# Kernel tuning notes

Hardware: AMD Instinct MI355X
Metric: run time of the kernel (lower is better)

Reference implementation:

```python
import jax, jax.numpy as jnp
import numpy as np

Bb, H, L = 4, 512, 4096      # batch, d_model, seq len
N2 = 32                       # d_state//2 complex conjugate-pair modes
Cch = 1                       # channels
DM = 512                      # d_model (output dim)

def setup_inputs() -> dict:
    key = jax.random.key(0)
    ks = jax.random.split(key, 8)
    u = jax.random.normal(ks[0], (Bb, H, L), jnp.float32)
    # dt ~ LogUniform[1e-3, 1e-1] as in S4 defaults
    log_dt = (jax.random.uniform(ks[1], (H,), jnp.float32)
              * (np.log(0.1) - np.log(0.001)) + np.log(0.001)).astype(jnp.float32)
    # S4D-Lin initialization: A = -1/2 + i*pi*n
    A_re = -0.5 * jnp.ones((H, N2), jnp.float32)
    A_im = jnp.broadcast_to(np.pi * jnp.arange(N2, dtype=np.float32), (H, N2)).astype(jnp.float32)
    B_re = jnp.ones((H, N2), jnp.float32)
    B_im = jnp.zeros((H, N2), jnp.float32)
    C_re = jax.random.normal(ks[2], (Cch, H, N2), jnp.float32) * (N2 ** -0.5)
    C_im = jax.random.normal(ks[3], (Cch, H, N2), jnp.float32) * (N2 ** -0.5)
    D = jax.random.normal(ks[4], (Cch, H), jnp.float32)
    W_out = jax.random.normal(ks[5], (2 * DM, Cch * H), jnp.float32) * ((Cch * H) ** -0.5)
    b_out = jnp.zeros((2 * DM,), jnp.float32)
    return {"u": u, "log_dt": log_dt, "A_re": A_re, "A_im": A_im,
            "B_re": B_re, "B_im": B_im, "C_re": C_re, "C_im": C_im,
            "D": D, "W_out": W_out, "b_out": b_out}

def reference(u, log_dt, A_re, A_im, B_re, B_im, C_re, C_im, D, W_out, b_out):
    # --- SSM kernel generation (diag / S4D, ZOH discretization) ---
    dt = jnp.exp(log_dt)                      # (H,)
    A = A_re + 1j * A_im                      # (H, N2)
    Bc = B_re + 1j * B_im                     # (H, N2)
    Cc = C_re + 1j * C_im                     # (C, H, N2)
    dtA = dt[:, None] * A                     # (H, N2)
    dB = (jnp.exp(dtA) - 1.0) / A * Bc        # (H, N2)
    pos = jnp.arange(L, dtype=jnp.float32)
    V = jnp.exp(dtA[:, :, None] * pos)        # (H, N2, L) Vandermonde of dA^l
    # factor 2 accounts for conjugate-pair halves
    k = (2.0 * jnp.einsum('chn,hn,hnl->chl', Cc, dB, V).real).astype(u.dtype)  # (C,H,L)
    # --- FFT convolution: y = k * u (causal, linear conv via zero-padded FFT) ---
    n_fft = 2 * L
    k_f = jnp.fft.rfft(k, n=n_fft)            # (C, H, L+1)
    u_f = jnp.fft.rfft(u, n=n_fft)            # (B, H, L+1)
    y_f = jnp.einsum('bhl,chl->bchl', u_f, k_f)
    y = jnp.fft.irfft(y_f, n=n_fft)[..., :L]  # (B, C, H, L)
    # skip connection D
    y = y + jnp.einsum('bhl,ch->bchl', u, D)
    y = y.reshape(u.shape[0], Cch * H, L)     # 'b c h l -> b (c h) l'
    # pointwise activation (exact GELU, matching torch default)
    y = jax.nn.gelu(y, approximate=False)
    # output linear (transposed, kernel-size-1) + GLU over channel dim
    z = jnp.einsum('bhl,oh->bol', y, W_out) + b_out[None, :, None]  # (B, 2*DM, L)
    out = z[:, :DM] * jax.nn.sigmoid(z[:, DM:])                      # (B, DM, L)
    return out
```

## Files before the change

### kernel.cpp

```cpp
#include <hip/hip_runtime.h>
#include <math.h>

#define BB 4
#define HH 512
#define LL 4096
#define NN 32
#define DMOUT 512

typedef __attribute__((ext_vector_type(8))) short short8;
typedef __attribute__((ext_vector_type(4))) float f32x4;

__device__ __forceinline__ unsigned f2bf(float x) {
    unsigned u = __float_as_uint(x);
    return (u + 0x7fffu + ((u >> 16) & 1u)) >> 16;
}
__device__ __forceinline__ unsigned packhl(float x) {
    unsigned hb = f2bf(x);
    float xh = __uint_as_float(hb << 16);
    return (hb << 16) | f2bf(x - xh);
}
__device__ __forceinline__ float reconhl(unsigned v) {
    return __uint_as_float(v & 0xffff0000u) + __uint_as_float(v << 16);
}
__device__ __forceinline__ void gload_lds16(const void* g, void* l) {
    __builtin_amdgcn_global_load_lds((const __attribute__((address_space(1))) void*)g,
                                     (__attribute__((address_space(3))) void*)l, 16, 0, 0);
}

__global__ void wsplit_kernel(const float* __restrict__ W, unsigned short* __restrict__ whi) {
    int i = (blockIdx.x * 256 + threadIdx.x) * 4;
    float4 w = *(const float4*)(W + i);
    ushort4 o;
    o.x = (unsigned short)f2bf(w.x);
    o.y = (unsigned short)f2bf(w.y);
    o.z = (unsigned short)f2bf(w.z);
    o.w = (unsigned short)f2bf(w.w);
    *(ushort4*)(whi + i) = o;
}

__global__ __launch_bounds__(256) void prep_kernel(
    const float* __restrict__ log_dt,
    const float* __restrict__ A_re, const float* __restrict__ A_im,
    const float* __restrict__ B_re, const float* __restrict__ B_im,
    const float* __restrict__ C_re, const float* __restrict__ C_im,
    unsigned* __restrict__ A3t, unsigned* __restrict__ Et) {
    const int h = blockIdx.x;
    const int tid = threadIdx.x;
    __shared__ float cst_lds[256];

    if (tid < 32) {
        int n = tid;
        float dt = expf(log_dt[h]);
        float ar = A_re[h * NN + n], ai = A_im[h * NN + n];
        float dtar = dt * ar, dtai = dt * ai;
        float ea = expf(dtar);
        float s, c; sincosf(dtai, &s, &c);
        float dA_r = ea * c, dA_i = ea * s;
        float em_r = dA_r - 1.0f, em_i = dA_i;
        float inv = 1.0f / (ar * ar + ai * ai);
        float t_r = (em_r * ar + em_i * ai) * inv;
        float t_i = (em_i * ar - em_r * ai) * inv;
        float br = B_re[h * NN + n], bi = B_im[h * NN + n];
        cst_lds[0 * 32 + n] = dtar;
        cst_lds[1 * 32 + n] = dtai;
        cst_lds[2 * 32 + n] = dA_r;
        cst_lds[3 * 32 + n] = dA_i;
        cst_lds[4 * 32 + n] = t_r * br - t_i * bi;
        cst_lds[5 * 32 + n] = t_r * bi + t_i * br;
        cst_lds[6 * 32 + n] = 2.0f * C_re[h * NN + n];
        cst_lds[7 * 32 + n] = 2.0f * C_im[h * NN + n];
    }
    __syncthreads();

    const int n = tid & 31, q = tid >> 5;
    const float dtar = cst_lds[0 * 32 + n], dtai = cst_lds[1 * 32 + n];
    const float dAr = cst_lds[2 * 32 + n], dAi = cst_lds[3 * 32 + n];
    const float dbr = cst_lds[4 * 32 + n], dbi = cst_lds[5 * 32 + n];
    const float tcr = cst_lds[6 * 32 + n], tci = cst_lds[7 * 32 + n];

    {
        float p = (float)(56 - q * 8);
        float mr = expf(p * dtar);
        float s, c; sincosf(p * dtai, &s, &c);
        float pr = mr * c, pi = mr * s;
        unsigned* base = A3t + (size_t)h * 4096;
#pragma unroll
        for (int jj = 7; jj >= 0; jj--) {
            int m = q * 8 + jj;
            base[m * 64 + n]      = packhl(dbr * pr - dbi * pi);
            base[m * 64 + 32 + n] = packhl(dbr * pi + dbi * pr);
            float nr2 = pr * dAr - pi * dAi;
            pi = pr * dAi + pi * dAr;
            pr = nr2;
        }
    }
    {
        float p = (float)(q * 8 + 1);
        float mr = expf(p * dtar);
        float s, c; sincosf(p * dtai, &s, &c);
        float pr = mr * c, pi = mr * s;
        unsigned* base = Et + (size_t)h * 4096;
#pragma unroll
        for (int i = q * 8; i <= q * 8 + 7; i++) {
            base[i * 64 + n]      = packhl(tcr * pr - tci * pi);
            base[i * 64 + 32 + n] = packhl(-(tcr * pi + tci * pr));
            float nr2 = pr * dAr - pi * dAi;
            pi = pr * dAi + pi * dAr;
            pr = nr2;
        }
    }
}

__global__ __launch_bounds__(256, 4) void ssm_kernel(
    const float* __restrict__ u, const float* __restrict__ log_dt,
    const float* __restrict__ A_re, const float* __restrict__ A_im,
    const float* __restrict__ B_re, const float* __restrict__ B_im,
    const float* __restrict__ C_re, const float* __restrict__ C_im,
    const float* __restrict__ D,
    const unsigned* __restrict__ A3t, const unsigned* __restrict__ Et,
    unsigned short* __restrict__ yhi) {
    const int h = blockIdx.x;
    const int b = blockIdx.y;
    const int tid = threadIdx.x;
    const int lane = tid & 63;
    const int w = tid >> 6;
    const int g = lane >> 4;
    const int l15 = lane & 15;

    __shared__ unsigned short uh[64 * 72];
    __shared__ unsigned short ul[64 * 72];
    __shared__ unsigned XsR[32 * 65];
    __shared__ unsigned XsI[32 * 65];
    __shared__ unsigned karr_pk[128];
    __shared__ float kpart[256];
    __shared__ float cst_lds[256];

    {
        const float* urow = u + ((size_t)(b * HH + h)) * LL;
#pragma unroll
        for (int r = 0; r < 4; r++) {
            int f = tid + 256 * r;
            float4 v = *(const float4*)(urow + f * 4);
            int t = f >> 4, mb = (f & 15) << 2;
            unsigned hx = f2bf(v.x), hy = f2bf(v.y), hz = f2bf(v.z), hw = f2bf(v.w);
            uint2 hwv;
            hwv.x = hx | (hy << 16);
            hwv.y = hz | (hw << 16);
            float rx = v.x - __uint_as_float(hx << 16);
            float ry = v.y - __uint_as_float(hy << 16);
            float rz = v.z - __uint_as_float(hz << 16);
            float rw = v.w - __uint_as_float(hw << 16);
            uint2 lwv;
            lwv.x = f2bf(rx) | (f2bf(ry) << 16);
            lwv.y = f2bf(rz) | (f2bf(rw) << 16);
            *(uint2*)(&uh[t * 72 + mb]) = hwv;
            *(uint2*)(&ul[t * 72 + mb]) = lwv;
        }
    }
    if (tid < 32) {
        int n = tid;
        float dt = expf(log_dt[h]);
        float ar = A_re[h * NN + n], ai = A_im[h * NN + n];
        float dtar = dt * ar, dtai = dt * ai;
        float ea = expf(dtar);
        float s, c; sincosf(dtai, &s, &c);
        float dA_r = ea * c, dA_i = ea * s;
        float em_r = dA_r - 1.0f, em_i = dA_i;
        float inv = 1.0f / (ar * ar + ai * ai);
        float t_r = (em_r * ar + em_i * ai) * inv;
        float t_i = (em_i * ar - em_r * ai) * inv;
        float br = B_re[h * NN + n], bi = B_im[h * NN + n];
        cst_lds[0 * 32 + n] = dtar;
        cst_lds[1 * 32 + n] = dtai;
        cst_lds[2 * 32 + n] = dA_r;
        cst_lds[3 * 32 + n] = dA_i;
        cst_lds[4 * 32 + n] = t_r * br - t_i * bi;
        cst_lds[5 * 32 + n] = t_r * bi + t_i * br;
        cst_lds[6 * 32 + n] = 2.0f * C_re[h * NN + n];
        cst_lds[7 * 32 + n] = 2.0f * C_im[h * NN + n];
    }
    __syncthreads();

    {
        int nprime = w * 16 + l15;
        const unsigned* a3b = A3t + (size_t)h * 4096 + nprime;
        short8 a3h0, a3l0, a3h1, a3l1;
#pragma unroll
        for (int j = 0; j < 8; j++) {
            unsigned v = a3b[(g * 8 + j) * 64];
            a3h0[j] = (short)(v >> 16); a3l0[j] = (short)(v & 0xffffu);
            unsigned v2 = a3b[(32 + g * 8 + j) * 64];
            a3h1[j] = (short)(v2 >> 16); a3l1[j] = (short)(v2 & 0xffffu);
        }
#pragma unroll
        for (int ni = 0; ni < 4; ni++) {
            int t = ni * 16 + l15;
            short8 uH0 = *(const short8*)(uh + t * 72 + g * 8);
            short8 uL0 = *(const short8*)(ul + t * 72 + g * 8);
            short8 uH1 = *(const short8*)(uh + t * 72 + 32 + g * 8);
            short8 uL1 = *(const short8*)(ul + t * 72 + 32 + g * 8);
            f32x4 a = (f32x4){0.f, 0.f, 0.f, 0.f};
            a = __builtin_amdgcn_mfma_f32_16x16x32_bf16(a3h0, uH0, a, 0, 0, 0);
            a = __builtin_amdgcn_mfma_f32_16x16x32_bf16(a3l0, uH0, a, 0, 0, 0);
            a = __builtin_amdgcn_mfma_f32_16x16x32_bf16(a3h0, uL0, a, 0, 0, 0);
            a = __builtin_amdgcn_mfma_f32_16x16x32_bf16(a3h1, uH1, a, 0, 0, 0);
            a = __builtin_amdgcn_mfma_f32_16x16x32_bf16(a3l1, uH1, a, 0, 0, 0);
            a = __builtin_amdgcn_mfma_f32_16x16x32_bf16(a3h1, uL1, a, 0, 0, 0);
            int nprime2 = w * 16 + g * 4;
#pragma unroll
            for (int r = 0; r < 4; r++) {
                int nn2 = nprime2 + r;
                if (nn2 < 32) XsR[nn2 * 65 + t] = __float_as_uint(a[r]);
                else          XsI[(nn2 - 32) * 65 + t] = __float_as_uint(a[r]);
            }
        }
    }
    {
        int j = tid & 63, nr = tid >> 6;
        float acc = 0.0f;
        if (j == 0) {
#pragma unroll
            for (int q = 0; q < 8; q++) {
                int n = nr * 8 + q;
                acc = fmaf(cst_lds[6 * 32 + n], cst_lds[4 * 32 + n], acc);
                acc = fmaf(-cst_lds[7 * 32 + n], cst_lds[5 * 32 + n], acc);
            }
        } else {
            const unsigned* eb = Et + (size_t)h * 4096 + (j - 1) * 64;
#pragma unroll
            for (int q = 0; q < 8; q++) {
                int n = nr * 8 + q;
                acc = fmaf(reconhl(eb[n]), cst_lds[4 * 32 + n], acc);
                acc = fmaf(reconhl(eb[32 + n]), cst_lds[5 * 32 + n], acc);
            }
        }
        kpart[nr * 64 + j] = acc;
    }
    __syncthreads();

    if (tid < 32) {
        int n = tid;
        float dtar = cst_lds[0 * 32 + n], dtai = cst_lds[1 * 32 + n];
        float mr = expf(64.0f * dtar);
        float s, c; sincosf(64.0f * dtai, &s, &c);
        float Mr = mr * c, Mi = mr * s;
        float cr = 0.f, ci = 0.f;
        unsigned* pR = XsR + n * 65;
        unsigned* pI = XsI + n * 65;
        float fr = __uint_as_float(pR[0]);
        float fi2 = __uint_as_float(pI[0]);
#pragma unroll 4
        for (int t = 0; t < 64; t++) {
            float frn = 0.f, fin = 0.f;
            if (t < 63) { frn = __uint_as_float(pR[t + 1]); fin = __uint_as_float(pI[t + 1]); }
            pR[t] = packhl(cr);
            pI[t] = packhl(ci);
            float nr = fmaf(Mr, cr, fmaf(-Mi, ci, fr));
            float nic = fmaf(Mr, ci, fmaf(Mi, cr, fi2));
            cr = nr; ci = nic;
            fr = frn; fi2 = fin;
        }
    } else if (tid >= 64 && tid < 128) {
        int j = tid - 64;
        float k = kpart[j] + kpart[64 + j] + kpart[128 + j] + kpart[192 + j];
        karr_pk[64 + j] = packhl(k);
    } else if (tid >= 128 && tid < 192) {
        karr_pk[tid - 128] = 0u;
    }
    __syncthreads();

    {
        int i = w * 16 + l15;
        short8 kh0, kl0, kh1, kl1;
#pragma unroll
        for (int j = 0; j < 8; j++) {
            unsigned v0 = karr_pk[64 + i - (g * 8 + j)];
            kh0[j] = (short)(v0 >> 16); kl0[j] = (short)(v0 & 0xffffu);
            unsigned v1 = karr_pk[64 + i - (32 + g * 8 + j)];
            kh1[j] = (short)(v1 >> 16); kl1[j] = (short)(v1 & 0xffffu);
        }
        short8 e0h, e0l, e1h, e1l;
        {
            const unsigned* eb = Et + (size_t)h * 4096 + i * 64;
#pragma unroll
            for (int j = 0; j < 8; j++) {
                int n = g * 8 + j;
                unsigned v = eb[n];
                e0h[j] = (short)(v >> 16); e0l[j] = (short)(v & 0xffffu);
                unsigned v2 = eb[32 + n];
                e1h[j] = (short)(v2 >> 16); e1l[j] = (short)(v2 & 0xffffu);
            }
        }
        float Dh = D[h];
        unsigned short* orow = yhi + ((size_t)(b * HH + h)) * LL;
#pragma unroll
        for (int ni = 0; ni < 4; ni++) {
            int t = ni * 16 + l15;
            short8 uH0 = *(const short8*)(uh + t * 72 + g * 8);
            short8 uL0 = *(const short8*)(ul + t * 72 + g * 8);
            short8 uH1 = *(const short8*)(uh + t * 72 + 32 + g * 8);
            short8 uL1 = *(const short8*)(ul + t * 72 + 32 + g * 8);
            short8 xrh, xrl, xih, xil;
#pragma unroll
            for (int j = 0; j < 8; j++) {
                unsigned v = XsR[(g * 8 + j) * 65 + t];
                xrh[j] = (short)(v >> 16); xrl[j] = (short)(v & 0xffffu);
                unsigned v2 = XsI[(g * 8 + j) * 65 + t];
                xih[j] = (short)(v2 >> 16); xil[j] = (short)(v2 & 0xffffu);
            }
            f32x4 a = (f32x4){0.f, 0.f, 0.f, 0.f};
            a = __builtin_amdgcn_mfma_f32_16x16x32_bf16(kh0, uH0, a, 0, 0, 0);
            a = __builtin_amdgcn_mfma_f32_16x16x32_bf16(kl0, uH0, a, 0, 0, 0);
            a = __builtin_amdgcn_mfma_f32_16x16x32_bf16(kh0, uL0, a, 0, 0, 0);
            a = __builtin_amdgcn_mfma_f32_16x16x32_bf16(kh1, uH1, a, 0, 0, 0);
            a = __builtin_amdgcn_mfma_f32_16x16x32_bf16(kl1, uH1, a, 0, 0, 0);
            a = __builtin_amdgcn_mfma_f32_16x16x32_bf16(kh1, uL1, a, 0, 0, 0);
            a = __builtin_amdgcn_mfma_f32_16x16x32_bf16(e0h, xrh, a, 0, 0, 0);
            a = __builtin_amdgcn_mfma_f32_16x16x32_bf16(e0h, xrl, a, 0, 0, 0);
            a = __builtin_amdgcn_mfma_f32_16x16x32_bf16(e0l, xrh, a, 0, 0, 0);
            a = __builtin_amdgcn_mfma_f32_16x16x32_bf16(e1h, xih, a, 0, 0, 0);
            a = __builtin_amdgcn_mfma_f32_16x16x32_bf16(e1h, xil, a, 0, 0, 0);
            a = __builtin_amdgcn_mfma_f32_16x16x32_bf16(e1l, xih, a, 0, 0, 0);
            ushort4 ov;
            unsigned short* op = &ov.x;
#pragma unroll
            for (int r = 0; r < 4; r++) {
                int io = w * 16 + g * 4 + r;
                float uv = __uint_as_float(((unsigned)uh[t * 72 + io]) << 16)
                         + __uint_as_float(((unsigned)ul[t * 72 + io]) << 16);
                float y = a[r] + Dh * uv;
                float gl = 0.5f * y * (1.0f + erff(y * 0.70710678118654752f));
                op[r] = (unsigned short)f2bf(gl);
            }
            *(ushort4*)(&orow[t * 64 + w * 16 + g * 4]) = ov;
        }
    }
}

__global__ __launch_bounds__(256) void gemm_glu_mfma(const unsigned short* __restrict__ yhi,
                                                     const float* __restrict__ W,
                                                     const unsigned short* __restrict__ whi,
                                                     const float* __restrict__ bias,
                                                     float* __restrict__ out, int preW) {
    const int b = blockIdx.z;
    const int d0 = blockIdx.y * 64;
    const int l0 = blockIdx.x * 64;
    const int tid = threadIdx.x;
    const int lane = tid & 63;
    const int wid = tid >> 6;
    const int wave_m = wid & 1;
    const int wave_n = wid >> 1;
    const int l15 = lane & 15;
    const int g = lane >> 4;

    __shared__ unsigned short Ysh[32 * 64];
    __shared__ char Wlds[128 * 64];

    f32x4 acc[4][2];
#pragma unroll
    for (int i = 0; i < 4; i++)
#pragma unroll
        for (int j = 0; j < 2; j++) acc[i][j] = (f32x4){0.f, 0.f, 0.f, 0.f};

    for (int kt = 0; kt < 16; kt++) {
        const int h0 = kt * 32;
        __syncthreads();
        {
            int kr = tid >> 3;
            int cc = tid & 7;
            int scol = (cc * 8) ^ ((kr & 8) ? 8 : 0);
            const unsigned short* src = yhi + ((size_t)(b * HH + h0 + kr)) * LL + l0 + scol;
            gload_lds16(src, (char*)Ysh + tid * 16);
        }
        if (preW) {
#pragma unroll
            for (int e = 0; e < 2; e++) {
                int c = e * 256 + tid;
                int row = c >> 2;
                int gx = c & 3;
                int qq = (row >> 1) & 3;
                int grow = (row < 64) ? (d0 + row) : (448 + d0 + row);
                const unsigned short* src = whi + (size_t)grow * 512 + h0 + ((gx ^ qq) * 8);
                gload_lds16(src, Wlds + c * 16);
            }
        } else {
            int row = tid >> 1;
            int kb = (tid & 1) * 16;
            int qq = (row >> 1) & 3;
            int grow = (row < 64) ? (d0 + row) : (448 + d0 + row);
            const float* src = W + (size_t)grow * 512 + h0 + kb;
            float4 w0 = *(const float4*)(src);
            float4 w1 = *(const float4*)(src + 4);
            float4 w2 = *(const float4*)(src + 8);
            float4 w3 = *(const float4*)(src + 12);
            short8 v0, v1;
            v0[0] = (short)f2bf(w0.x); v0[1] = (short)f2bf(w0.y);
            v0[2] = (short)f2bf(w0.z); v0[3] = (short)f2bf(w0.w);
            v0[4] = (short)f2bf(w1.x); v0[5] = (short)f2bf(w1.y);
            v0[6] = (short)f2bf(w1.z); v0[7] = (short)f2bf(w1.w);
            v1[0] = (short)f2bf(w2.x); v1[1] = (short)f2bf(w2.y);
            v1[2] = (short)f2bf(w2.z); v1[3] = (short)f2bf(w2.w);
            v1[4] = (short)f2bf(w3.x); v1[5] = (short)f2bf(w3.y);
            v1[6] = (short)f2bf(w3.z); v1[7] = (short)f2bf(w3.w);
            int g0 = kb >> 3;
            *(short8*)(Wlds + row * 64 + ((g0 ^ qq) * 16)) = v0;
            *(short8*)(Wlds + row * 64 + (((g0 + 1) ^ qq) * 16)) = v1;
        }
        __syncthreads();

        short8 af[4];
#pragma unroll
        for (int mi = 0; mi < 4; mi++) {
            int rowb = (mi < 2) ? (wave_m * 32 + mi * 16) : (64 + wave_m * 32 + (mi - 2) * 16);
            int row = rowb + l15;
            int qq = (row >> 1) & 3;
            af[mi] = *(const short8*)(Wlds + row * 64 + ((g ^ qq) * 16));
        }
#pragma unroll
        for (int ni = 0; ni < 2; ni++) {
            int col = wave_n * 32 + ni * 16 + l15;
            int cs = col ^ ((g & 1) << 3);
            const unsigned short* yb = Ysh + (8 * g) * 64 + cs;
            short8 bh;
            bh[0] = (short)yb[0 * 64];
            bh[1] = (short)yb[1 * 64];
            bh[2] = (short)yb[2 * 64];
            bh[3] = (short)yb[3 * 64];
            bh[4] = (short)yb[4 * 64];
            bh[5] = (short)yb[5 * 64];
            bh[6] = (short)yb[6 * 64];
            bh[7] = (short)yb[7 * 64];
#pragma unroll
            for (int mi = 0; mi < 4; mi++) {
                acc[mi][ni] = __builtin_amdgcn_mfma_f32_16x16x32_bf16(af[mi], bh, acc[mi][ni], 0, 0, 0);
            }
        }
    }

#pragma unroll
    for (int mi = 0; mi < 2; mi++) {
        int dbase = d0 + wave_m * 32 + mi * 16 + (g << 2);
#pragma unroll
        for (int r = 0; r < 4; r++) {
            int d = dbase + r;
            float b1 = bias[d], b2 = bias[DMOUT + d];
#pragma unroll
            for (int ni = 0; ni < 2; ni++) {
                int l = l0 + wave_n * 32 + ni * 16 + l15;
                float z1 = acc[mi][ni][r] + b1;
                float z2 = acc[mi + 2][ni][r] + b2;
                out[((size_t)(b * DMOUT + d)) * LL + l] = z1 * (1.0f / (1.0f + expf(-z2)));
            }
        }
    }
}

extern "C" void kernel_launch(void* const* d_in, const int* in_sizes, int n_in,
                              void* d_out, int out_size, void* d_ws, size_t ws_size,
                              hipStream_t stream) {
    const float* u      = (const float*)d_in[0];
    const float* log_dt = (const float*)d_in[1];
    const float* A_re   = (const float*)d_in[2];
    const float* A_im   = (const float*)d_in[3];
    const float* B_re   = (const float*)d_in[4];
    const float* B_im   = (const float*)d_in[5];
    const float* C_re   = (const float*)d_in[6];
    const float* C_im   = (const float*)d_in[7];
    const float* D      = (const float*)d_in[8];
    const float* W      = (const float*)d_in[9];
    const float* bias   = (const float*)d_in[10];
    float* out = (float*)d_out;

    char* ws = (char*)d_ws;
    unsigned short* yhi = (unsigned short*)ws;
    unsigned* A3t = (unsigned*)(ws + 16777216);
    unsigned* Et  = (unsigned*)(ws + 16777216 + 8388608);
    unsigned short* whi = (unsigned short*)(ws + 33554432);
    int preW = (ws_size >= (size_t)(33554432 + 1048576)) ? 1 : 0;

    if (preW) wsplit_kernel<<<512, 256, 0, stream>>>(W, whi);
    prep_kernel<<<HH, 256, 0, stream>>>(log_dt, A_re, A_im, B_re, B_im, C_re, C_im, A3t, Et);
    ssm_kernel<<<dim3(HH, BB), 256, 0, stream>>>(u, log_dt, A_re, A_im, B_re, B_im,
                                                 C_re, C_im, D, A3t, Et, yhi);
    gemm_glu_mfma<<<dim3(64, 8, BB), 256, 0, stream>>>(yhi, W, whi, bias, out, preW);
}
```

Baseline: 92.32 us.

## Double-buffer GEMM LDS tiles, fold W conversion into prep, hoist Et loads

The GEMM+GLU kernel now double-buffers its Y and W shared-memory tiles, issuing the next k-tile's async global-to-LDS loads before computing on the current one, with one barrier per iteration instead of two. The separate W-to-bf16 conversion kernel is merged into prep_kernel, which saves one launch. In the SSM kernel, the Et fragment loads are hoisted above a barrier so their latency overlaps other work. The cost is doubled LDS use in the GEMM, which may lower occupancy, and more live registers in the SSM kernel.

```diff
diff --git a/kernel.cpp b/kernel.cpp
--- a/kernel.cpp
+++ b/kernel.cpp
@@ -27,26 +27,28 @@
                                      (__attribute__((address_space(3))) void*)l, 16, 0, 0);
 }
 
-__global__ void wsplit_kernel(const float* __restrict__ W, unsigned short* __restrict__ whi) {
-    int i = (blockIdx.x * 256 + threadIdx.x) * 4;
-    float4 w = *(const float4*)(W + i);
-    ushort4 o;
-    o.x = (unsigned short)f2bf(w.x);
-    o.y = (unsigned short)f2bf(w.y);
-    o.z = (unsigned short)f2bf(w.z);
-    o.w = (unsigned short)f2bf(w.w);
-    *(ushort4*)(whi + i) = o;
-}
-
 __global__ __launch_bounds__(256) void prep_kernel(
     const float* __restrict__ log_dt,
     const float* __restrict__ A_re, const float* __restrict__ A_im,
     const float* __restrict__ B_re, const float* __restrict__ B_im,
     const float* __restrict__ C_re, const float* __restrict__ C_im,
-    unsigned* __restrict__ A3t, unsigned* __restrict__ Et) {
+    const float* __restrict__ W,
+    unsigned* __restrict__ A3t, unsigned* __restrict__ Et,
+    unsigned short* __restrict__ whi, int preW) {
     const int h = blockIdx.x;
     const int tid = threadIdx.x;
     __shared__ float cst_lds[256];
+
+    if (preW) {
+        int i = (h * 256 + tid) * 4;
+        float4 wv = *(const float4*)(W + i);
+        ushort4 o;
+        o.x = (unsigned short)f2bf(wv.x);
+        o.y = (unsigned short)f2bf(wv.y);
+        o.z = (unsigned short)f2bf(wv.z);
+        o.w = (unsigned short)f2bf(wv.w);
+        *(ushort4*)(whi + i) = o;
+    }
 
     if (tid < 32) {
         int n = tid;
@@ -236,6 +238,19 @@
         }
         kpart[nr * 64 + j] = acc;
     }
+    short8 e0h, e0l, e1h, e1l;
+    {
+        int i = w * 16 + l15;
+        const unsigned* eb = Et + (size_t)h * 4096 + i * 64;
+#pragma unroll
+        for (int j = 0; j < 8; j++) {
+            int n = g * 8 + j;
+            unsigned v = eb[n];
+            e0h[j] = (short)(v >> 16); e0l[j] = (short)(v & 0xffffu);
+            unsigned v2 = eb[32 + n];
+            e1h[j] = (short)(v2 >> 16); e1l[j] = (short)(v2 & 0xffffu);
+        }
+    }
     __syncthreads();
 
     if (tid < 32) {
@@ -279,18 +294,6 @@
             unsigned v1 = karr_pk[64 + i - (32 + g * 8 + j)];
             kh1[j] = (short)(v1 >> 16); kl1[j] = (short)(v1 & 0xffffu);
         }
-        short8 e0h, e0l, e1h, e1l;
-        {
-            const unsigned* eb = Et + (size_t)h * 4096 + i * 64;
-#pragma unroll
-            for (int j = 0; j < 8; j++) {
-                int n = g * 8 + j;
-                unsigned v = eb[n];
-                e0h[j] = (short)(v >> 16); e0l[j] = (short)(v & 0xffffu);
-                unsigned v2 = eb[32 + n];
-                e1h[j] = (short)(v2 >> 16); e1l[j] = (short)(v2 & 0xffffu);
-            }
-        }
         float Dh = D[h];
         unsigned short* orow = yhi + ((size_t)(b * HH + h)) * LL;
 #pragma unroll
@@ -353,8 +356,8 @@
     const int l15 = lane & 15;
     const int g = lane >> 4;
 
-    __shared__ unsigned short Ysh[32 * 64];
-    __shared__ char Wlds[128 * 64];
+    __shared__ unsigned short Ysh[2][32 * 64];
+    __shared__ char Wlds[2][128 * 64];
 
     f32x4 acc[4][2];
 #pragma unroll
@@ -362,51 +365,58 @@
 #pragma unroll
         for (int j = 0; j < 2; j++) acc[i][j] = (f32x4){0.f, 0.f, 0.f, 0.f};
 
+#define STAGE(BUF, KT)                                                                   \
+    {                                                                                    \
+        const int h0s = (KT) * 32;                                                       \
+        {                                                                                \
+            int kr = tid >> 3;                                                           \
+            int cc = tid & 7;                                                            \
+            int scol = (cc * 8) ^ ((kr & 8) ? 8 : 0);                                    \
+            const unsigned short* srcY = yhi + ((size_t)(b * HH + h0s + kr)) * LL + l0 + scol; \
+            gload_lds16(srcY, (char*)Ysh[BUF] + tid * 16);                               \
+        }                                                                                \
+        if (preW) {                                                                      \
+            _Pragma("unroll")                                                            \
+            for (int e = 0; e < 2; e++) {                                                \
+                int c = e * 256 + tid;                                                   \
+                int row = c >> 2;                                                        \
+                int gx = c & 3;                                                          \
+                int qq = (row >> 1) & 3;                                                 \
+                int grow = (row < 64) ? (d0 + row) : (448 + d0 + row);                   \
+                const unsigned short* srcW = whi + (size_t)grow * 512 + h0s + ((gx ^ qq) * 8); \
+                gload_lds16(srcW, Wlds[BUF] + c * 16);                                   \
+            }                                                                            \
+        } else {                                                                         \
+            int row = tid >> 1;                                                          \
+            int kb = (tid & 1) * 16;                                                     \
+            int qq = (row >> 1) & 3;                                                     \
+            int grow = (row < 64) ? (d0 + row) : (448 + d0 + row);                       \
+            const float* srcW = W + (size_t)grow * 512 + h0s + kb;                       \
+            float4 w0 = *(const float4*)(srcW);                                          \
+            float4 w1 = *(const float4*)(srcW + 4);                                      \
+            float4 w2 = *(const float4*)(srcW + 8);                                      \
+            float4 w3 = *(const float4*)(srcW + 12);                                     \
+            short8 v0, v1;                                                               \
+            v0[0] = (short)f2bf(w0.x); v0[1] = (short)f2bf(w0.y);                        \
+            v0[2] = (short)f2bf(w0.z); v0[3] = (short)f2bf(w0.w);                        \
+            v0[4] = (short)f2bf(w1.x); v0[5] = (short)f2bf(w1.y);                        \
+            v0[6] = (short)f2bf(w1.z); v0[7] = (short)f2bf(w1.w);                        \
+            v1[0] = (short)f2bf(w2.x); v1[1] = (short)f2bf(w2.y);                        \
+            v1[2] = (short)f2bf(w2.z); v1[3] = (short)f2bf(w2.w);                        \
+            v1[4] = (short)f2bf(w3.x); v1[5] = (short)f2bf(w3.y);                        \
+            v1[6] = (short)f2bf(w3.z); v1[7] = (short)f2bf(w3.w);                        \
+            int g0 = kb >> 3;                                                            \
+            *(short8*)(Wlds[BUF] + row * 64 + ((g0 ^ qq) * 16)) = v0;                    \
+            *(short8*)(Wlds[BUF] + row * 64 + (((g0 + 1) ^ qq) * 16)) = v1;              \
+        }                                                                                \
+    }
+
+    STAGE(0, 0)
+    __syncthreads();
+
+    int cur = 0;
     for (int kt = 0; kt < 16; kt++) {
-        const int h0 = kt * 32;
-        __syncthreads();
-        {
-            int kr = tid >> 3;
-            int cc = tid & 7;
-            int scol = (cc * 8) ^ ((kr & 8) ? 8 : 0);
-            const unsigned short* src = yhi + ((size_t)(b * HH + h0 + kr)) * LL + l0 + scol;
-            gload_lds16(src, (char*)Ysh + tid * 16);
-        }
-        if (preW) {
-#pragma unroll
-            for (int e = 0; e < 2; e++) {
-                int c = e * 256 + tid;
-                int row = c >> 2;
-                int gx = c & 3;
-                int qq = (row >> 1) & 3;
-                int grow = (row < 64) ? (d0 + row) : (448 + d0 + row);
-                const unsigned short* src = whi + (size_t)grow * 512 + h0 + ((gx ^ qq) * 8);
-                gload_lds16(src, Wlds + c * 16);
-            }
-        } else {
-            int row = tid >> 1;
-            int kb = (tid & 1) * 16;
-            int qq = (row >> 1) & 3;
-            int grow = (row < 64) ? (d0 + row) : (448 + d0 + row);
-            const float* src = W + (size_t)grow * 512 + h0 + kb;
-            float4 w0 = *(const float4*)(src);
-            float4 w1 = *(const float4*)(src + 4);
-            float4 w2 = *(const float4*)(src + 8);
-            float4 w3 = *(const float4*)(src + 12);
-            short8 v0, v1;
-            v0[0] = (short)f2bf(w0.x); v0[1] = (short)f2bf(w0.y);
-            v0[2] = (short)f2bf(w0.z); v0[3] = (short)f2bf(w0.w);
-            v0[4] = (short)f2bf(w1.x); v0[5] = (short)f2bf(w1.y);
-            v0[6] = (short)f2bf(w1.z); v0[7] = (short)f2bf(w1.w);
-            v1[0] = (short)f2bf(w2.x); v1[1] = (short)f2bf(w2.y);
-            v1[2] = (short)f2bf(w2.z); v1[3] = (short)f2bf(w2.w);
-            v1[4] = (short)f2bf(w3.x); v1[5] = (short)f2bf(w3.y);
-            v1[6] = (short)f2bf(w3.z); v1[7] = (short)f2bf(w3.w);
-            int g0 = kb >> 3;
-            *(short8*)(Wlds + row * 64 + ((g0 ^ qq) * 16)) = v0;
-            *(short8*)(Wlds + row * 64 + (((g0 + 1) ^ qq) * 16)) = v1;
-        }
-        __syncthreads();
+        if (kt < 15) STAGE(cur ^ 1, kt + 1)
 
         short8 af[4];
 #pragma unroll
@@ -414,13 +424,13 @@
             int rowb = (mi < 2) ? (wave_m * 32 + mi * 16) : (64 + wave_m * 32 + (mi - 2) * 16);
             int row = rowb + l15;
             int qq = (row >> 1) & 3;
-            af[mi] = *(const short8*)(Wlds + row * 64 + ((g ^ qq) * 16));
+            af[mi] = *(const short8*)(Wlds[cur] + row * 64 + ((g ^ qq) * 16));
         }
 #pragma unroll
         for (int ni = 0; ni < 2; ni++) {
             int col = wave_n * 32 + ni * 16 + l15;
             int cs = col ^ ((g & 1) << 3);
-            const unsigned short* yb = Ysh + (8 * g) * 64 + cs;
+            const unsigned short* yb = Ysh[cur] + (8 * g) * 64 + cs;
             short8 bh;
             bh[0] = (short)yb[0 * 64];
             bh[1] = (short)yb[1 * 64];
@@ -435,7 +445,10 @@
                 acc[mi][ni] = __builtin_amdgcn_mfma_f32_16x16x32_bf16(af[mi], bh, acc[mi][ni], 0, 0, 0);
             }
         }
-    }
+        __syncthreads();
+        cur ^= 1;
+    }
+#undef STAGE
 
 #pragma unroll
     for (int mi = 0; mi < 2; mi++) {
@@ -478,8 +491,8 @@
     unsigned short* whi = (unsigned short*)(ws + 33554432);
     int preW = (ws_size >= (size_t)(33554432 + 1048576)) ? 1 : 0;
 
-    if (preW) wsplit_kernel<<<512, 256, 0, stream>>>(W, whi);
-    prep_kernel<<<HH, 256, 0, stream>>>(log_dt, A_re, A_im, B_re, B_im, C_re, C_im, A3t, Et);
+    prep_kernel<<<HH, 256, 0, stream>>>(log_dt, A_re, A_im, B_re, B_im, C_re, C_im,
+                                        W, A3t, Et, whi, preW);
     ssm_kernel<<<dim3(HH, BB), 256, 0, stream>>>(u, log_dt, A_re, A_im, B_re, B_im,
                                                  C_re, C_im, D, A3t, Et, yhi);
     gemm_glu_mfma<<<dim3(64, 8, BB), 256, 0, stream>>>(yhi, W, whi, bias, out, preW);
```

After: 88.53 us. -4.1%, faster.
